# Performance work log

Hardware: AMD Instinct MI355X
Metric: run time of the kernel (lower is better)

Reference implementation:

```python
import jax, jax.numpy as jnp
import numpy as np

STRIDE = 2
F_SCALE = 4


def _layer_norm(x, eps=1e-5):
    # F.layer_norm over the last 3 dims (C,H,W), no affine
    m = jnp.mean(x, axis=(1, 2, 3), keepdims=True)
    v = jnp.var(x, axis=(1, 2, 3), keepdims=True)
    return (x - m) * jax.lax.rsqrt(v + eps)


def _conv(x, w, b, dil, pad):
    y = jax.lax.conv_general_dilated(
        x, w, window_strides=(1, 1), padding=[(pad, pad), (pad, pad)],
        rhs_dilation=(dil, dil), dimension_numbers=('NCHW', 'OIHW', 'NCHW'))
    return y + b[None, :, None, None]


def _unshuffle(x, f):
    # [B,C,H,W] -> [B*f*f, C, H/f, W/f]; sub-image k=dy*f+dx samples offsets (dy,dx) stride f
    B, C, H, W = x.shape
    sh, sw = H // f, W // f
    x = x.reshape(B, C, sh, f, sw, f)
    x = x.transpose(0, 3, 5, 1, 2, 4)  # [B, dy, dx, C, sh, sw]
    return x.reshape(B * f * f, C, sh, sw)


def _shuffle(x, B, f):
    # inverse of _unshuffle: [B*f*f, C, sh, sw] -> [B, C, sh*f, sw*f]
    _, C, sh, sw = x.shape
    x = x.reshape(B, f, f, C, sh, sw)
    x = x.transpose(0, 3, 4, 1, 5, 2)  # [B, C, sh, dy, sw, dx]
    return x.reshape(B, C, sh * f, sw * f)


def _attention(x, wqk, f):
    B, C, H, W = x.shape
    E = wqk.shape[1]
    ph, pw = (-H) % f, (-W) % f
    xx = _layer_norm(x)
    if ph or pw:
        xx = jnp.pad(xx, ((0, 0), (0, 0), (0, ph), (0, pw)))
        xp = jnp.pad(x, ((0, 0), (0, 0), (0, ph), (0, pw)))
    else:
        xp = x
    sub = _unshuffle(xx, f)   # [Bf, C, sh, sw]
    v = _unshuffle(xp, f)     # [Bf, C, sh, sw]
    Bf, _, sh, sw = sub.shape
    N = sh * sw
    q = sub.transpose(0, 2, 3, 1).reshape(Bf, N, C)
    vf = v.transpose(0, 2, 3, 1).reshape(Bf, N, C)
    qk = jnp.einsum('bnc,ce->bne', q, wqk)
    qk = qk / (jnp.linalg.norm(qk, axis=-1, keepdims=True) + 1e-8)
    attn = (jnp.einsum('bne,bme->bnm', qk, qk) + 1.0) / np.sqrt(E).astype(np.float32)
    attn = jax.nn.softmax(attn, axis=-1)
    out = jnp.einsum('bnm,bmc->bnc', attn, vf)
    out = out.reshape(Bf, sh, sw, C).transpose(0, 3, 1, 2)
    out = _shuffle(out, B, f)
    return out[:, :, :H, :W]


def setup_inputs() -> dict:
    key = jax.random.key(0)
    ks = jax.random.split(key, 8)
    B, C, H, W = 2, 128, 192, 192
    E = C  # ss_exp_factor = 1.0
    x = jax.random.normal(ks[0], (B, C, H, W), jnp.float32)
    lim = 1.414 * np.sqrt(6.0 / (C + E))  # xavier_uniform, gain=1.414
    wqk = jax.random.uniform(ks[1], (C, E), jnp.float32, -lim, lim)
    s = np.sqrt(2.0 / (C * 9)).astype(np.float32)
    w1 = jax.random.normal(ks[2], (C, C, 3, 3), jnp.float32) * s
    b1 = jnp.zeros((C,), jnp.float32)
    w2 = jax.random.normal(ks[3], (C, C, 3, 3), jnp.float32) * s
    b2 = jnp.zeros((C,), jnp.float32)
    w3 = jax.random.normal(ks[4], (C, C, 1, 1), jnp.float32) * np.sqrt(2.0 / C).astype(np.float32)
    b3 = jnp.zeros((C,), jnp.float32)
    return {"x": x, "wqk": wqk, "w1": w1, "b1": b1, "w2": w2, "b2": b2, "w3": w3, "b3": b3}


def reference(x, wqk, w1, b1, w2, b2, w3, b3):
    f = F_SCALE * STRIDE
    y = x + _attention(x, wqk, f)
    h = jax.nn.relu(_conv(y, w1, b1, STRIDE, STRIDE))
    h = jax.nn.relu(_conv(h, w2, b2, STRIDE, STRIDE))
    h = _conv(h, w3, b3, 1, 0)
    return x + h
```

## Files before the change

kernel.cpp:

```cpp
#include <hip/hip_runtime.h>
#include <math.h>

#define CCH 128
#define HH 192
#define WW 192
#define BB 2
#define HW (HH*WW)
#define CHW (CCH*HW)
#define BF 128
#define NN 576
#define SH 24

typedef __attribute__((ext_vector_type(8))) short short8;
typedef __attribute__((ext_vector_type(4))) float floatx4;
typedef unsigned int uint32;
typedef unsigned short ushort;

__device__ __forceinline__ unsigned short bf16r(float f) {
    uint32 u = __float_as_uint(f);
    u += 0x7fffu + ((u >> 16) & 1u);
    return (unsigned short)(u >> 16);
}

__global__ __launch_bounds__(256) void k_reduce(const float* __restrict__ x, float* __restrict__ stats) {
    int b = blockIdx.y;
    const float4* p = (const float4*)(x + (size_t)b*CHW) + (size_t)blockIdx.x*4096;
    float s = 0.f, sq = 0.f;
#pragma unroll
    for (int k = 0; k < 16; ++k) {
        float4 v = p[threadIdx.x + 256*k];
        s  += v.x + v.y + v.z + v.w;
        sq += v.x*v.x + v.y*v.y + v.z*v.z + v.w*v.w;
    }
    for (int off = 32; off; off >>= 1) { s += __shfl_down(s, off); sq += __shfl_down(sq, off); }
    __shared__ float ls[4], lq[4];
    int wave = threadIdx.x >> 6, lane = threadIdx.x & 63;
    if (lane == 0) { ls[wave] = s; lq[wave] = sq; }
    __syncthreads();
    if (threadIdx.x == 0) {
        atomicAdd(&stats[2*b],   ls[0]+ls[1]+ls[2]+ls[3]);
        atomicAdd(&stats[2*b+1], lq[0]+lq[1]+lq[2]+lq[3]);
    }
}

__global__ void k_finalize(float* stats) {
    int b = threadIdx.x;
    if (b < BB) {
        float s = stats[2*b], sq = stats[2*b+1];
        float mean = s / (float)CHW;
        float var = sq / (float)CHW - mean*mean;
        stats[4 + 2*b] = mean;
        stats[5 + 2*b] = rsqrtf(var + 1e-5f);
    }
}

__global__ __launch_bounds__(256) void k_unshuffle(const float* __restrict__ x, const float* __restrict__ stats,
                                                   ushort* __restrict__ Vt, ushort* __restrict__ Xnb) {
    __shared__ float t[128][65];
    int x0 = blockIdx.x * 64;
    int y  = blockIdx.y;
    int b  = blockIdx.z;
    float mean = stats[4+2*b], istd = stats[5+2*b];
    const float* src = x + (size_t)b*CHW + (size_t)y*WW + x0;
#pragma unroll
    for (int k = 0; k < 32; ++k) {
        int idx = threadIdx.x + 256*k;
        int c = idx >> 6, xl = idx & 63;
        t[c][xl] = src[(size_t)c*HW + xl];
    }
    __syncthreads();
    int i = y >> 3, dy = y & 7;
#pragma unroll
    for (int k = 0; k < 32; ++k) {
        int idx = threadIdx.x + 256*k;
        int xl = idx & 63, c = idx >> 6;
        int xx = x0 + xl;
        int j = xx >> 3, dx = xx & 7;
        int bf = (b << 6) + (dy << 3) + dx;
        int n = i*SH + j;
        Vt[((size_t)bf*CCH + c)*NN + n] = bf16r(t[c][xl]);
    }
#pragma unroll
    for (int k = 0; k < 16; ++k) {
        int idx = threadIdx.x + 256*k;
        int c2 = idx & 63, xl = idx >> 6;
        int c = c2 * 2;
        int xx = x0 + xl;
        int j = xx >> 3, dx = xx & 7;
        int bf = (b << 6) + (dy << 3) + dx;
        int n = i*SH + j;
        float v0 = (t[c][xl]   - mean) * istd;
        float v1 = (t[c+1][xl] - mean) * istd;
        uint32 p = (uint32)bf16r(v0) | ((uint32)bf16r(v1) << 16);
        *(uint32*)&Xnb[((size_t)bf*NN + n)*CCH + c] = p;
    }
}

__global__ __launch_bounds__(256, 4) void k_qk(const ushort* __restrict__ Xnb, const ushort* __restrict__ wqkTb,
                                               ushort* __restrict__ qkn) {
    __shared__ ushort Bs[128*136];
    int bid = blockIdx.x;
    int bf = bid / 9, tile = bid % 9;
    int n0 = tile * 64;
    int tid = threadIdx.x;
    int wv = tid >> 6, l = tid & 63, quad = l >> 4, l15 = l & 15;
    {
        const uint4* bsrc = (const uint4*)wqkTb;
#pragma unroll
        for (int k = 0; k < 8; ++k) {
            int idx = tid + 256*k;
            int row = idx >> 4, co = idx & 15;
            *(uint4*)&Bs[row*136 + co*8] = bsrc[idx];
        }
    }
    int qb = wv*16;
    const ushort* arow = Xnb + ((size_t)bf*NN + n0 + qb + l15)*CCH + quad*8;
    short8 a[4];
#pragma unroll
    for (int kk = 0; kk < 4; ++kk)
        a[kk] = *(const short8*)(arow + kk*32);
    __syncthreads();
    floatx4 acc[8];
#pragma unroll
    for (int nt = 0; nt < 8; ++nt) acc[nt] = (floatx4){0.f,0.f,0.f,0.f};
#pragma unroll
    for (int kk = 0; kk < 4; ++kk)
#pragma unroll
        for (int nt = 0; nt < 8; ++nt) {
            const short8 bfr = *(const short8*)&Bs[(nt*16 + l15)*136 + kk*32 + quad*8];
            acc[nt] = __builtin_amdgcn_mfma_f32_16x16x32_bf16(a[kk], bfr, acc[nt], 0, 0, 0);
        }
    float ss[4] = {0.f,0.f,0.f,0.f};
#pragma unroll
    for (int nt = 0; nt < 8; ++nt)
#pragma unroll
        for (int r = 0; r < 4; ++r) ss[r] += acc[nt][r]*acc[nt][r];
#pragma unroll
    for (int off = 1; off < 16; off <<= 1)
#pragma unroll
        for (int r = 0; r < 4; ++r) ss[r] += __shfl_xor(ss[r], off);
    float fr[4];
#pragma unroll
    for (int r = 0; r < 4; ++r) fr[r] = 1.f / (sqrtf(ss[r]) + 1e-8f);
    __syncthreads();
    ushort* mys = &Bs[qb*128];
#pragma unroll
    for (int nt = 0; nt < 8; ++nt)
#pragma unroll
        for (int r = 0; r < 4; ++r)
            mys[(quad*4 + r)*128 + nt*16 + l15] = bf16r(acc[nt][r]*fr[r]);
    uint4* dst = (uint4*)(qkn + ((size_t)bf*NN + n0 + qb)*CCH);
    const uint4* ls = (const uint4*)mys;
#pragma unroll
    for (int k = 0; k < 4; ++k)
        dst[l + 64*k] = ls[l + 64*k];
}

__global__ __launch_bounds__(384, 4) void k_attn(const ushort* __restrict__ qkn, const ushort* __restrict__ Vt_g,
                                                 float* __restrict__ O) {
    __shared__ ushort Ks[64*136];
    __shared__ ushort Vs[128*72];
    __shared__ ushort Ps[96*76];
    int id = blockIdx.x;
    int bfl = id & 7, widx = id >> 3;
    int tile = widx % 6;
    int bf = ((widx / 6) << 3) | bfl;
    int n0 = tile*96;
    int tid = threadIdx.x;
    int wv = tid >> 6, l = tid & 63, quad = l >> 4, l15 = l & 15;
    int qb = wv*16;

    const uint4* kv_base = (const uint4*)(qkn + (size_t)bf*NN*CCH);
    const uint4* vsrc = (const uint4*)(Vt_g + (size_t)bf*CCH*NN);

    const ushort* qrow = qkn + ((size_t)bf*NN + n0 + qb + l15)*CCH + quad*8;
    short8 aq[4];
#pragma unroll
    for (int kk = 0; kk < 4; ++kk)
        aq[kk] = *(const short8*)(qrow + kk*32);

    floatx4 oacc[8];
#pragma unroll
    for (int ct = 0; ct < 8; ++ct) oacc[ct] = (floatx4){0.f,0.f,0.f,0.f};
    float rsum[4] = {0.f,0.f,0.f,0.f};
    const float scale = 0.08838834764831845f;

    for (int mt = 0; mt < 9; ++mt) {
        __syncthreads();
        {
            const uint4* ks = kv_base + (size_t)mt*1024;
            int mo8 = mt*8;
#pragma unroll
            for (int k = 0; k < 3; ++k) {
                int idx = tid + 384*k;
                if (idx < 1024)
                    *(uint4*)&Ks[(idx >> 4)*136 + (idx & 15)*8] = ks[idx];
            }
#pragma unroll
            for (int k = 0; k < 3; ++k) {
                int idx = tid + 384*k;
                if (idx < 1024)
                    *(uint4*)&Vs[(idx >> 3)*72 + (idx & 7)*8] = vsrc[(size_t)(idx >> 3)*72 + mo8 + (idx & 7)];
            }
        }
        __syncthreads();

        floatx4 sc[4];
#pragma unroll
        for (int t = 0; t < 4; ++t) sc[t] = (floatx4){0.f,0.f,0.f,0.f};
        __builtin_amdgcn_s_setprio(1);
#pragma unroll
        for (int kk = 0; kk < 4; ++kk)
#pragma unroll
            for (int t = 0; t < 4; ++t) {
                const short8 bk = *(const short8*)&Ks[(t*16 + l15)*136 + kk*32 + quad*8];
                sc[t] = __builtin_amdgcn_mfma_f32_16x16x32_bf16(aq[kk], bk, sc[t], 0, 0, 0);
            }
        __builtin_amdgcn_s_setprio(0);

        float pr[4] = {0.f,0.f,0.f,0.f};
#pragma unroll
        for (int t = 0; t < 4; ++t)
#pragma unroll
            for (int r = 0; r < 4; ++r) {
                float p = __expf((sc[t][r] + 1.f)*scale);
                Ps[(qb + quad*4 + r)*76 + t*16 + l15] = bf16r(p);
                pr[r] += p;
            }
#pragma unroll
        for (int off = 1; off < 16; off <<= 1)
#pragma unroll
            for (int r = 0; r < 4; ++r) pr[r] += __shfl_xor(pr[r], off);
#pragma unroll
        for (int r = 0; r < 4; ++r) rsum[r] += pr[r];

        short8 ap[2];
        ap[0] = *(const short8*)&Ps[(qb + l15)*76 + quad*8];
        ap[1] = *(const short8*)&Ps[(qb + l15)*76 + 32 + quad*8];
        __builtin_amdgcn_s_setprio(1);
#pragma unroll
        for (int ct = 0; ct < 8; ++ct)
#pragma unroll
            for (int kk2 = 0; kk2 < 2; ++kk2) {
                const short8 bv = *(const short8*)&Vs[(ct*16 + l15)*72 + kk2*32 + quad*8];
                oacc[ct] = __builtin_amdgcn_mfma_f32_16x16x32_bf16(ap[kk2], bv, oacc[ct], 0, 0, 0);
            }
        __builtin_amdgcn_s_setprio(0);
    }

    float rinv[4];
#pragma unroll
    for (int r = 0; r < 4; ++r) rinv[r] = 1.f / rsum[r];
#pragma unroll
    for (int ct = 0; ct < 8; ++ct)
#pragma unroll
        for (int r = 0; r < 4; ++r)
            O[((size_t)bf*NN + n0 + qb + quad*4 + r)*CCH + ct*16 + l15] = oacc[ct][r]*rinv[r];
}

__global__ __launch_bounds__(256) void k_shuffle_add(const float* __restrict__ O, const float* __restrict__ x,
                                                     uint4* __restrict__ yb) {
    __shared__ float t[128][65];
    int x0 = blockIdx.x * 64;
    int yy = blockIdx.y;
    int b  = blockIdx.z;
    if (blockIdx.x == 0 && threadIdx.x < 64) {
        int oct = threadIdx.x >> 2, p = threadIdx.x & 3;
        int col = (p < 2) ? p : 192 + p;
        uint4 z; z.x = 0; z.y = 0; z.z = 0; z.w = 0;
        yb[((size_t)(b*192 + yy)*16 + oct)*196 + col] = z;
    }
    int i = yy >> 3, dy = yy & 7;
#pragma unroll
    for (int k = 0; k < 32; ++k) {
        int idx = threadIdx.x + 256*k;
        int c = idx & 127, xl = idx >> 7;
        int xx = x0 + xl;
        int j = xx >> 3, dx = xx & 7;
        int bf = (b << 6) + (dy << 3) + dx;
        int n = i*SH + j;
        t[c][xl] = O[((size_t)bf*NN + n)*CCH + c];
    }
    __syncthreads();
    size_t base = (size_t)b*CHW + (size_t)yy*WW + x0;
#pragma unroll
    for (int k = 0; k < 32; ++k) {
        int idx = threadIdx.x + 256*k;
        int c = idx >> 6, xl = idx & 63;
        t[c][xl] += x[base + (size_t)c*HW + xl];
    }
    __syncthreads();
#pragma unroll
    for (int k = 0; k < 4; ++k) {
        int idx = threadIdx.x + 256*k;
        int xl = idx & 63, oc = idx >> 6;
        uint32 d[4];
#pragma unroll
        for (int j = 0; j < 4; ++j) {
            float f0 = t[oc*8 + 2*j][xl];
            float f1 = t[oc*8 + 2*j + 1][xl];
            d[j] = (uint32)bf16r(f0) | ((uint32)bf16r(f1) << 16);
        }
        uint4 v; v.x = d[0]; v.y = d[1]; v.z = d[2]; v.w = d[3];
        yb[((size_t)(b*192 + yy)*16 + oc)*196 + (x0 + xl + 2)] = v;
    }
}

__global__ __launch_bounds__(256) void k_cast_w(const float* __restrict__ w1, const float* __restrict__ w2,
                                                const float* __restrict__ w3, const float* __restrict__ wqk,
                                                uint4* __restrict__ wb1, uint4* __restrict__ wb2,
                                                uint4* __restrict__ w3b, uint4* __restrict__ wqkTb) {
    int id = blockIdx.x*256 + threadIdx.x;
    if (blockIdx.y == 2) {
        if (id < 2048) {
            int co = id >> 4, oct = id & 15;
            uint32 r[4];
#pragma unroll
            for (int j = 0; j < 4; ++j) {
                float f0 = w3[(size_t)co*128 + oct*8 + 2*j];
                float f1 = w3[(size_t)co*128 + oct*8 + 2*j + 1];
                r[j] = (uint32)bf16r(f0) | ((uint32)bf16r(f1) << 16);
            }
            uint4 v; v.x = r[0]; v.y = r[1]; v.z = r[2]; v.w = r[3];
            w3b[id] = v;
            int e = co;
            uint32 r2[4];
#pragma unroll
            for (int j = 0; j < 4; ++j) {
                float f0 = wqk[(size_t)(oct*8 + 2*j)*128 + e];
                float f1 = wqk[(size_t)(oct*8 + 2*j + 1)*128 + e];
                r2[j] = (uint32)bf16r(f0) | ((uint32)bf16r(f1) << 16);
            }
            uint4 v2; v2.x = r2[0]; v2.y = r2[1]; v2.z = r2[2]; v2.w = r2[3];
            wqkTb[id] = v2;
        }
        return;
    }
    const float* w = (blockIdx.y == 0) ? w1 : w2;
    uint4* wb = (blockIdx.y == 0) ? wb1 : wb2;
    int co = id & 127;
    int oct = (id >> 7) & 3;
    int chunk = (id >> 9) & 3;
    int tap = id >> 11;
    int ci0 = chunk*32 + oct*8;
    uint32 r[4];
#pragma unroll
    for (int j = 0; j < 4; ++j) {
        float f0 = w[(size_t)(co*128 + ci0 + 2*j)*9 + tap];
        float f1 = w[(size_t)(co*128 + ci0 + 2*j + 1)*9 + tap];
        r[j] = (uint32)bf16r(f0) | ((uint32)bf16r(f1) << 16);
    }
    uint4 v; v.x = r[0]; v.y = r[1]; v.z = r[2]; v.w = r[3];
    wb[((size_t)(tap*4 + chunk)*4 + oct)*128 + co] = v;
}

__global__ __launch_bounds__(256, 3) void k_conv3m(const uint4* __restrict__ yb, const uint4* __restrict__ wb,
                                                   const float* __restrict__ bias, void* __restrict__ outp,
                                                   int mode) {
    __shared__ uint4 As[864];
    __shared__ uint4 Ws[2][512];
    int xt = blockIdx.x;
    int rg = blockIdx.y;
    int b  = blockIdx.z;
    int par = rg & 1, g = rg >> 1;
    int y0 = 8*g + par;
    int x0 = xt*32;
    int tid = threadIdx.x;
    int wv = tid >> 6, l = tid & 63, quad = l >> 4, l15 = l & 15;
    int yw = y0 + 2*wv;

    if (mode == 0 && xt == 0) {
        int rowp = y0 + 2*(tid >> 6);
        int oct = (tid >> 2) & 15, p = tid & 3;
        int col = (p < 2) ? p : 192 + p;
        uint4 z; z.x = 0; z.y = 0; z.z = 0; z.w = 0;
        ((uint4*)outp)[((size_t)(b*192 + rowp)*16 + oct)*196 + col] = z;
    }

    floatx4 acc[2][8];
#pragma unroll
    for (int mt = 0; mt < 2; ++mt)
#pragma unroll
        for (int nt = 0; nt < 8; ++nt) acc[mt][nt] = (floatx4){0.f,0.f,0.f,0.f};

    const uint4* ybb = yb + (size_t)b*602112;

    for (int chunk = 0; chunk < 4; ++chunk) {
        __syncthreads();
#pragma unroll
        for (int k = 0; k < 4; ++k) {
            int idx = tid + 256*k;
            if (idx < 864) {
                int r = idx / 144;
                int rem = idx - r*144;
                int oct = rem / 36;
                int px = rem - oct*36;
                int grow = y0 - 2 + 2*r;
                uint4 v; v.x = 0; v.y = 0; v.z = 0; v.w = 0;
                if (grow >= 0 && grow < 192)
                    v = ybb[((size_t)grow*16 + chunk*4 + oct)*196 + x0 + px];
                As[idx] = v;
            }
        }
        {
            const uint4* src = wb + (size_t)chunk*512;
            Ws[0][tid]     = src[tid];
            Ws[0][tid+256] = src[tid+256];
        }
        __syncthreads();
#pragma unroll
        for (int tap = 0; tap < 9; ++tap) {
            if (tap < 8) {
                const uint4* src = wb + (size_t)((tap+1)*4 + chunk)*512;
                Ws[(tap+1)&1][tid]     = src[tid];
                Ws[(tap+1)&1][tid+256] = src[tid+256];
            }
            const int ky = tap/3, kx = tap - 3*(tap/3);
            int r = wv + ky;
            const short8 a0 = *(const short8*)&As[(r*4 + quad)*36 + l15 + 2*kx];
            const short8 a1 = *(const short8*)&As[(r*4 + quad)*36 + 16 + l15 + 2*kx];
            const uint4* wbuf = &Ws[tap&1][0];
#pragma unroll
            for (int nt = 0; nt < 8; ++nt) {
                const short8 bf = *(const short8*)&wbuf[quad*128 + nt*16 + l15];
                acc[0][nt] = __builtin_amdgcn_mfma_f32_16x16x32_bf16(a0, bf, acc[0][nt], 0, 0, 0);
                acc[1][nt] = __builtin_amdgcn_mfma_f32_16x16x32_bf16(a1, bf, acc[1][nt], 0, 0, 0);
            }
            __syncthreads();
        }
    }

    if (mode == 0) {
        unsigned short* outb = (unsigned short*)outp;
#pragma unroll
        for (int nt = 0; nt < 8; ++nt) {
            int co = nt*16 + l15;
            float bv = bias[co];
            size_t base = (((size_t)(b*192 + yw)*16 + ((co>>5)*4 + ((co>>3)&3)))*196)*8 + (size_t)(co&7);
#pragma unroll
            for (int mt = 0; mt < 2; ++mt)
#pragma unroll
                for (int rr = 0; rr < 4; ++rr) {
                    int xx = x0 + mt*16 + quad*4 + rr;
                    float v = fmaxf(acc[mt][nt][rr] + bv, 0.f);
                    outb[base + (size_t)(xx+2)*8] = bf16r(v);
                }
        }
    } else {
        unsigned short* outb = (unsigned short*)outp;
#pragma unroll
        for (int nt = 0; nt < 8; ++nt) {
            int co = nt*16 + l15;
            float bv = bias[co];
#pragma unroll
            for (int mt = 0; mt < 2; ++mt)
#pragma unroll
                for (int rr = 0; rr < 4; ++rr) {
                    int xx = x0 + mt*16 + quad*4 + rr;
                    float v = fmaxf(acc[mt][nt][rr] + bv, 0.f);
                    outb[((size_t)b*36864 + (size_t)yw*192 + xx)*128 + co] = bf16r(v);
                }
        }
    }
}

__global__ __launch_bounds__(256, 2) void k_conv1x1m(const ushort* __restrict__ h2b, const uint4* __restrict__ w3b,
                                                     const float* __restrict__ b3, const float* __restrict__ x,
                                                     float* __restrict__ out) {
    __shared__ ushort Hs[128*136];
    __shared__ ushort Ws3[128*136];
    int px0 = blockIdx.x * 128;
    int b = blockIdx.y;
    int tid = threadIdx.x;
    int wv = tid >> 6, l = tid & 63, quad = l >> 4, l15 = l & 15;

    {
        const uint4* hsrc = (const uint4*)(h2b + ((size_t)b*36864 + px0)*128);
#pragma unroll
        for (int k = 0; k < 8; ++k) {
            int idx = tid + 256*k;
            int row = idx >> 4, co8 = idx & 15;
            *(uint4*)&Hs[row*136 + co8*8] = hsrc[idx];
            *(uint4*)&Ws3[row*136 + co8*8] = w3b[idx];
        }
    }
    __syncthreads();

    floatx4 oacc[2][8];
#pragma unroll
    for (int mt = 0; mt < 2; ++mt)
#pragma unroll
        for (int nt = 0; nt < 8; ++nt) oacc[mt][nt] = (floatx4){0.f,0.f,0.f,0.f};

#pragma unroll
    for (int kk = 0; kk < 4; ++kk) {
        const short8 aq0 = *(const short8*)&Hs[(wv*32 + l15)*136 + kk*32 + quad*8];
        const short8 aq1 = *(const short8*)&Hs[(wv*32 + 16 + l15)*136 + kk*32 + quad*8];
#pragma unroll
        for (int nt = 0; nt < 8; ++nt) {
            const short8 bw = *(const short8*)&Ws3[(nt*16 + l15)*136 + kk*32 + quad*8];
            oacc[0][nt] = __builtin_amdgcn_mfma_f32_16x16x32_bf16(aq0, bw, oacc[0][nt], 0, 0, 0);
            oacc[1][nt] = __builtin_amdgcn_mfma_f32_16x16x32_bf16(aq1, bw, oacc[1][nt], 0, 0, 0);
        }
    }

#pragma unroll
    for (int nt = 0; nt < 8; ++nt) {
        int co = nt*16 + l15;
        float bv = b3[co];
        size_t pbase = ((size_t)b*128 + co)*HW + px0 + wv*32 + quad*4;
#pragma unroll
        for (int mt = 0; mt < 2; ++mt) {
            const float4 xv = *(const float4*)&x[pbase + mt*16];
            float4 o;
            o.x = oacc[mt][nt][0] + bv + xv.x;
            o.y = oacc[mt][nt][1] + bv + xv.y;
            o.z = oacc[mt][nt][2] + bv + xv.z;
            o.w = oacc[mt][nt][3] + bv + xv.w;
            *(float4*)&out[pbase + mt*16] = o;
        }
    }
}

extern "C" void kernel_launch(void* const* d_in, const int* in_sizes, int n_in,
                              void* d_out, int out_size, void* d_ws, size_t ws_size,
                              hipStream_t stream) {
    (void)in_sizes; (void)n_in; (void)out_size; (void)ws_size;
    const float* x   = (const float*)d_in[0];
    const float* wqk = (const float*)d_in[1];
    const float* w1  = (const float*)d_in[2];
    const float* b1  = (const float*)d_in[3];
    const float* w2  = (const float*)d_in[4];
    const float* b2  = (const float*)d_in[5];
    const float* w3  = (const float*)d_in[6];
    const float* b3  = (const float*)d_in[7];
    float* out = (float*)d_out;
    char* ws = (char*)d_ws;
    float* stats = (float*)ws;
    const size_t SZ = (size_t)BF * NN * CCH * sizeof(float);
    char* Abase = ws + 256;
    char* Bbase = ws + 256 + SZ;
    char* Cbase = ws + 256 + 2*SZ;
    ushort* Vt  = (ushort*)Abase;
    ushort* Xnb = (ushort*)Bbase;
    ushort* qkn = (ushort*)Cbase;
    float*  O   = (float*)Bbase;
    uint4*  yb  = (uint4*)Cbase;
    uint4*  h1b = (uint4*)Abase;
    ushort* h2b = (ushort*)Bbase;
    uint4* wb1   = (uint4*)(Abase + 20*1024*1024);
    uint4* wb2   = (uint4*)(Abase + 21*1024*1024);
    uint4* w3b   = (uint4*)(Abase + 22*1024*1024);
    uint4* wqkTb = (uint4*)(Abase + 23*1024*1024);

    hipMemsetAsync(stats, 0, 4*sizeof(float), stream);
    k_reduce     <<<dim3(288, 2),     256, 0, stream>>>(x, stats);
    k_finalize   <<<1, 64,            0, stream>>>(stats);
    k_cast_w     <<<dim3(72, 3),      256, 0, stream>>>(w1, w2, w3, wqk, wb1, wb2, w3b, wqkTb);
    k_unshuffle  <<<dim3(3, 192, 2),  256, 0, stream>>>(x, stats, Vt, Xnb);
    k_qk         <<<1152,             256, 0, stream>>>(Xnb, (const ushort*)wqkTb, qkn);
    k_attn       <<<768,              384, 0, stream>>>(qkn, Vt, O);
    k_shuffle_add<<<dim3(3, 192, 2),  256, 0, stream>>>(O, x, yb);
    k_conv3m     <<<dim3(6, 48, 2),   256, 0, stream>>>(yb,  wb1, b1, (void*)h1b, 0);
    k_conv3m     <<<dim3(6, 48, 2),   256, 0, stream>>>(h1b, wb2, b2, (void*)h2b, 1);
    k_conv1x1m   <<<dim3(288, 2),     256, 0, stream>>>(h2b, w3b, b3, x, out);
}
```

Baseline: 311.9 us.

## Enlarge attention query tile to 192 rows with three query subtiles per wave

Each attention block now handles 192 query rows with 4 waves, and each wave processes three 16-row query subtiles that share every K and V fragment read from LDS. This halves the number of blocks and the total K/V reloads from global memory, and reuses each LDS-loaded B operand across three MFMAs. In exchange, per-thread register use grows considerably (three sets of accumulators and Q fragments), and launch bounds drop to 2 blocks per CU, so occupancy and latency hiding fall. With 384 blocks the grid may also fill the GPU less evenly.

```diff
diff --git a/kernel.cpp b/kernel.cpp
--- a/kernel.cpp
+++ b/kernel.cpp
@@ -156,33 +156,42 @@
         dst[l + 64*k] = ls[l + 64*k];
 }
 
-__global__ __launch_bounds__(384, 4) void k_attn(const ushort* __restrict__ qkn, const ushort* __restrict__ Vt_g,
+__global__ __launch_bounds__(256, 2) void k_attn(const ushort* __restrict__ qkn, const ushort* __restrict__ Vt_g,
                                                  float* __restrict__ O) {
     __shared__ ushort Ks[64*136];
     __shared__ ushort Vs[128*72];
-    __shared__ ushort Ps[96*76];
+    __shared__ ushort Ps[192*72];
     int id = blockIdx.x;
     int bfl = id & 7, widx = id >> 3;
-    int tile = widx % 6;
-    int bf = ((widx / 6) << 3) | bfl;
-    int n0 = tile*96;
+    int tile = widx % 3;
+    int bf = ((widx / 3) << 3) | bfl;
+    int n0 = tile*192;
     int tid = threadIdx.x;
     int wv = tid >> 6, l = tid & 63, quad = l >> 4, l15 = l & 15;
-    int qb = wv*16;
+    int qb = wv*48;
 
     const uint4* kv_base = (const uint4*)(qkn + (size_t)bf*NN*CCH);
     const uint4* vsrc = (const uint4*)(Vt_g + (size_t)bf*CCH*NN);
 
-    const ushort* qrow = qkn + ((size_t)bf*NN + n0 + qb + l15)*CCH + quad*8;
-    short8 aq[4];
-#pragma unroll
-    for (int kk = 0; kk < 4; ++kk)
-        aq[kk] = *(const short8*)(qrow + kk*32);
-
-    floatx4 oacc[8];
-#pragma unroll
-    for (int ct = 0; ct < 8; ++ct) oacc[ct] = (floatx4){0.f,0.f,0.f,0.f};
-    float rsum[4] = {0.f,0.f,0.f,0.f};
+    short8 aq[3][4];
+#pragma unroll
+    for (int qs = 0; qs < 3; ++qs) {
+        const ushort* qrow = qkn + ((size_t)bf*NN + n0 + qb + qs*16 + l15)*CCH + quad*8;
+#pragma unroll
+        for (int kk = 0; kk < 4; ++kk)
+            aq[qs][kk] = *(const short8*)(qrow + kk*32);
+    }
+
+    floatx4 oacc[3][8];
+#pragma unroll
+    for (int qs = 0; qs < 3; ++qs)
+#pragma unroll
+        for (int ct = 0; ct < 8; ++ct) oacc[qs][ct] = (floatx4){0.f,0.f,0.f,0.f};
+    float rsum[3][4];
+#pragma unroll
+    for (int qs = 0; qs < 3; ++qs)
+#pragma unroll
+        for (int r = 0; r < 4; ++r) rsum[qs][r] = 0.f;
     const float scale = 0.08838834764831845f;
 
     for (int mt = 0; mt < 9; ++mt) {
@@ -191,71 +200,84 @@
             const uint4* ks = kv_base + (size_t)mt*1024;
             int mo8 = mt*8;
 #pragma unroll
-            for (int k = 0; k < 3; ++k) {
-                int idx = tid + 384*k;
-                if (idx < 1024)
-                    *(uint4*)&Ks[(idx >> 4)*136 + (idx & 15)*8] = ks[idx];
-            }
-#pragma unroll
-            for (int k = 0; k < 3; ++k) {
-                int idx = tid + 384*k;
-                if (idx < 1024)
-                    *(uint4*)&Vs[(idx >> 3)*72 + (idx & 7)*8] = vsrc[(size_t)(idx >> 3)*72 + mo8 + (idx & 7)];
+            for (int k = 0; k < 4; ++k) {
+                int idx = tid + 256*k;
+                *(uint4*)&Ks[(idx >> 4)*136 + (idx & 15)*8] = ks[idx];
+            }
+#pragma unroll
+            for (int k = 0; k < 4; ++k) {
+                int idx = tid + 256*k;
+                *(uint4*)&Vs[(idx >> 3)*72 + (idx & 7)*8] = vsrc[(size_t)(idx >> 3)*72 + mo8 + (idx & 7)];
             }
         }
         __syncthreads();
 
-        floatx4 sc[4];
-#pragma unroll
-        for (int t = 0; t < 4; ++t) sc[t] = (floatx4){0.f,0.f,0.f,0.f};
+        floatx4 sc[3][4];
+#pragma unroll
+        for (int qs = 0; qs < 3; ++qs)
+#pragma unroll
+            for (int t = 0; t < 4; ++t) sc[qs][t] = (floatx4){0.f,0.f,0.f,0.f};
         __builtin_amdgcn_s_setprio(1);
 #pragma unroll
         for (int kk = 0; kk < 4; ++kk)
 #pragma unroll
             for (int t = 0; t < 4; ++t) {
                 const short8 bk = *(const short8*)&Ks[(t*16 + l15)*136 + kk*32 + quad*8];
-                sc[t] = __builtin_amdgcn_mfma_f32_16x16x32_bf16(aq[kk], bk, sc[t], 0, 0, 0);
+#pragma unroll
+                for (int qs = 0; qs < 3; ++qs)
+                    sc[qs][t] = __builtin_amdgcn_mfma_f32_16x16x32_bf16(aq[qs][kk], bk, sc[qs][t], 0, 0, 0);
             }
         __builtin_amdgcn_s_setprio(0);
 
-        float pr[4] = {0.f,0.f,0.f,0.f};
-#pragma unroll
-        for (int t = 0; t < 4; ++t)
-#pragma unroll
-            for (int r = 0; r < 4; ++r) {
-                float p = __expf((sc[t][r] + 1.f)*scale);
-                Ps[(qb + quad*4 + r)*76 + t*16 + l15] = bf16r(p);
-                pr[r] += p;
-            }
-#pragma unroll
-        for (int off = 1; off < 16; off <<= 1)
-#pragma unroll
-            for (int r = 0; r < 4; ++r) pr[r] += __shfl_xor(pr[r], off);
-#pragma unroll
-        for (int r = 0; r < 4; ++r) rsum[r] += pr[r];
-
-        short8 ap[2];
-        ap[0] = *(const short8*)&Ps[(qb + l15)*76 + quad*8];
-        ap[1] = *(const short8*)&Ps[(qb + l15)*76 + 32 + quad*8];
+#pragma unroll
+        for (int qs = 0; qs < 3; ++qs) {
+            float pr[4] = {0.f,0.f,0.f,0.f};
+#pragma unroll
+            for (int t = 0; t < 4; ++t)
+#pragma unroll
+                for (int r = 0; r < 4; ++r) {
+                    float p = __expf((sc[qs][t][r] + 1.f)*scale);
+                    Ps[(qb + qs*16 + quad*4 + r)*72 + t*16 + l15] = bf16r(p);
+                    pr[r] += p;
+                }
+#pragma unroll
+            for (int off = 1; off < 16; off <<= 1)
+#pragma unroll
+                for (int r = 0; r < 4; ++r) pr[r] += __shfl_xor(pr[r], off);
+#pragma unroll
+            for (int r = 0; r < 4; ++r) rsum[qs][r] += pr[r];
+        }
+
+        short8 ap[3][2];
+#pragma unroll
+        for (int qs = 0; qs < 3; ++qs) {
+            ap[qs][0] = *(const short8*)&Ps[(qb + qs*16 + l15)*72 + quad*8];
+            ap[qs][1] = *(const short8*)&Ps[(qb + qs*16 + l15)*72 + 32 + quad*8];
+        }
         __builtin_amdgcn_s_setprio(1);
 #pragma unroll
         for (int ct = 0; ct < 8; ++ct)
 #pragma unroll
             for (int kk2 = 0; kk2 < 2; ++kk2) {
                 const short8 bv = *(const short8*)&Vs[(ct*16 + l15)*72 + kk2*32 + quad*8];
-                oacc[ct] = __builtin_amdgcn_mfma_f32_16x16x32_bf16(ap[kk2], bv, oacc[ct], 0, 0, 0);
+#pragma unroll
+                for (int qs = 0; qs < 3; ++qs)
+                    oacc[qs][ct] = __builtin_amdgcn_mfma_f32_16x16x32_bf16(ap[qs][kk2], bv, oacc[qs][ct], 0, 0, 0);
             }
         __builtin_amdgcn_s_setprio(0);
     }
 
-    float rinv[4];
-#pragma unroll
-    for (int r = 0; r < 4; ++r) rinv[r] = 1.f / rsum[r];
-#pragma unroll
-    for (int ct = 0; ct < 8; ++ct)
-#pragma unroll
-        for (int r = 0; r < 4; ++r)
-            O[((size_t)bf*NN + n0 + qb + quad*4 + r)*CCH + ct*16 + l15] = oacc[ct][r]*rinv[r];
+#pragma unroll
+    for (int qs = 0; qs < 3; ++qs) {
+        float rinv[4];
+#pragma unroll
+        for (int r = 0; r < 4; ++r) rinv[r] = 1.f / rsum[qs][r];
+#pragma unroll
+        for (int ct = 0; ct < 8; ++ct)
+#pragma unroll
+            for (int r = 0; r < 4; ++r)
+                O[((size_t)bf*NN + n0 + qb + qs*16 + quad*4 + r)*CCH + ct*16 + l15] = oacc[qs][ct][r]*rinv[r];
+    }
 }
 
 __global__ __launch_bounds__(256) void k_shuffle_add(const float* __restrict__ O, const float* __restrict__ x,
@@ -559,7 +581,7 @@
     k_cast_w     <<<dim3(72, 3),      256, 0, stream>>>(w1, w2, w3, wqk, wb1, wb2, w3b, wqkTb);
     k_unshuffle  <<<dim3(3, 192, 2),  256, 0, stream>>>(x, stats, Vt, Xnb);
     k_qk         <<<1152,             256, 0, stream>>>(Xnb, (const ushort*)wqkTb, qkn);
-    k_attn       <<<768,              384, 0, stream>>>(qkn, Vt, O);
+    k_attn       <<<384,              256, 0, stream>>>(qkn, Vt, O);
     k_shuffle_add<<<dim3(3, 192, 2),  256, 0, stream>>>(O, x, yb);
     k_conv3m     <<<dim3(6, 48, 2),   256, 0, stream>>>(yb,  wb1, b1, (void*)h1b, 0);
     k_conv3m     <<<dim3(6, 48, 2),   256, 0, stream>>>(h1b, wb2, b2, (void*)h2b, 1);
```

After: 294.4 us, median of 2. -5.6%, faster.
